# Kernel tuning notes

Measured on AMD Instinct MI355X. Metric: run time of the kernel, lower is better.

Reference implementation:

```python
import jax, jax.numpy as jnp
import numpy as np

N, E, DIN, H, HEADS = 50000, 800000, 128, 64, 4


def setup_inputs() -> dict:
    key = jax.random.key(0)
    ks = jax.random.split(key, 12)

    def p(k, shape, fan_in):
        return jax.random.normal(k, shape, dtype=jnp.float32) / np.float32(np.sqrt(fan_in))

    return dict(
        x=jax.random.normal(ks[0], (N, DIN), dtype=jnp.float32),
        edge_index=jax.random.randint(ks[1], (2, E), 0, N, dtype=jnp.int32),
        # GCNConv(input_dim, hidden)
        W_gcn=p(ks[2], (DIN, H), DIN), b_gcn=jnp.zeros((H,), jnp.float32),
        # GATConv(hidden, hidden, heads=4, concat=True)
        W_gat=p(ks[3], (H, HEADS * H), H),
        att_src=p(ks[4], (HEADS, H), H), att_dst=p(ks[5], (HEADS, H), H),
        b_gat=jnp.zeros((HEADS * H,), jnp.float32),
        # SAGEConv(4*hidden, hidden): lin_l (neighbors, with bias), lin_r (root, no bias)
        W_sage_l=p(ks[6], (HEADS * H, H), HEADS * H), b_sage=jnp.zeros((H,), jnp.float32),
        W_sage_r=p(ks[7], (HEADS * H, H), HEADS * H),
        # edge-pair MLP: Linear(2*hidden, hidden) -> ReLU -> Linear(hidden, 1)
        W1=p(ks[8], (2 * H, H), 2 * H), b1=jnp.zeros((H,), jnp.float32),
        W2=p(ks[9], (H, 1), H), b2=jnp.zeros((1,), jnp.float32),
    )


def reference(x, edge_index, W_gcn, b_gcn, W_gat, att_src, att_dst, b_gat,
              W_sage_l, b_sage, W_sage_r, W1, b1, W2, b2):
    n = x.shape[0]
    src, dst = edge_index[0], edge_index[1]
    loop = jnp.arange(n, dtype=edge_index.dtype)
    # edges with self-loops appended (GCN and GAT add self-loops by default)
    s2 = jnp.concatenate([src, loop])
    d2 = jnp.concatenate([dst, loop])

    h = x @ W_gcn                                            # [N, H]
    deg = jax.ops.segment_sum(jnp.ones_like(d2, jnp.float32), d2, num_segments=n)
    dinv = jnp.where(deg > 0, jax.lax.rsqrt(jnp.maximum(deg, 1e-12)), 0.0)
    norm = dinv[s2] * dinv[d2]                               # [E+N]
    h = jax.ops.segment_sum(h[s2] * norm[:, None], d2, num_segments=n) + b_gcn
    h = jax.nn.relu(h)                                       # dropout: identity in eval

    # ---- GATConv (heads=4, concat=True, negative_slope=0.2) ----
    g = (h @ W_gat).reshape(n, HEADS, H)                     # [N, heads, C]
    a_s = jnp.sum(g * att_src, axis=-1)                      # [N, heads]
    a_d = jnp.sum(g * att_dst, axis=-1)
    e = jax.nn.leaky_relu(a_s[s2] + a_d[d2], 0.2)            # [E+N, heads]
    m = jax.ops.segment_max(e, d2, num_segments=n)           # per-target max (stable softmax)
    e = jnp.exp(e - m[d2])
    z = jax.ops.segment_sum(e, d2, num_segments=n)
    alpha = e / (z[d2] + 1e-16)                              # edge softmax over incoming edges
    g = jax.ops.segment_sum(g[s2] * alpha[:, :, None], d2, num_segments=n)
    g = jax.nn.relu(g.reshape(n, HEADS * H) + b_gat)

    # ---- SAGEConv (mean aggregation, root weight, no self-loops) ----
    nsum = jax.ops.segment_sum(g[src], dst, num_segments=n)
    cnt = jax.ops.segment_sum(jnp.ones_like(dst, jnp.float32), dst, num_segments=n)
    mean = nsum / jnp.maximum(cnt, 1.0)[:, None]
    s = jax.nn.relu(mean @ W_sage_l + b_sage + g @ W_sage_r)  # [N, H]

    # ---- edge-pair MLP + sigmoid ----
    ef = jnp.concatenate([s[src], s[dst]], axis=1)            # [E, 2H]
    pred = jax.nn.relu(ef @ W1 + b1) @ W2 + b2                # [E, 1]
    return jax.nn.sigmoid(pred[:, 0])
```

## Files before the change

kernel.cpp:

```cpp
#include <hip/hip_runtime.h>
#include <math.h>

typedef float v2f __attribute__((ext_vector_type(2)));
static __device__ __forceinline__ float4 f4s(float v){ return make_float4(v,v,v,v); }
static __device__ __forceinline__ float4 f4add(float4 a, float4 b){ return make_float4(a.x+b.x,a.y+b.y,a.z+b.z,a.w+b.w); }
static __device__ __forceinline__ float4 f4max(float4 a, float4 b){ return make_float4(fmaxf(a.x,b.x),fmaxf(a.y,b.y),fmaxf(a.z,b.z),fmaxf(a.w,b.w)); }
static __device__ __forceinline__ float4 f4scale(float4 a, float s){ return make_float4(a.x*s,a.y*s,a.z*s,a.w*s); }
static __device__ __forceinline__ float4 f4fma(float4 acc, float s, float4 b){
  acc.x += s*b.x; acc.y += s*b.y; acc.z += s*b.z; acc.w += s*b.w; return acc;
}
static __device__ __forceinline__ float4 f4relu(float4 a){ return f4max(a, f4s(0.f)); }
static __device__ __forceinline__ float4 f4leaky(float4 a){
  return make_float4(a.x>0.f?a.x:0.2f*a.x, a.y>0.f?a.y:0.2f*a.y, a.z>0.f?a.z:0.2f*a.z, a.w>0.f?a.w:0.2f*a.w);
}
static __device__ __forceinline__ float4 f4expf(float4 a){ return make_float4(__expf(a.x),__expf(a.y),__expf(a.z),__expf(a.w)); }
static __device__ __forceinline__ unsigned short f2bf(float f){
  unsigned int u = __float_as_uint(f);
  unsigned int r = (u + 0x7fffu + ((u >> 16) & 1u)) >> 16;
  return (unsigned short)r;
}
static __device__ __forceinline__ ushort4 f2bf4(float4 f){
  ushort4 r; r.x=f2bf(f.x); r.y=f2bf(f.y); r.z=f2bf(f.z); r.w=f2bf(f.w); return r;
}
static __device__ __forceinline__ float4 bfu2f4(uint2 u){
  return make_float4(__uint_as_float(u.x << 16), __uint_as_float(u.x & 0xffff0000u),
                     __uint_as_float(u.y << 16), __uint_as_float(u.y & 0xffff0000u));
}
static __device__ __forceinline__ float4 bfu2f4_lo(uint4 u){ return bfu2f4(make_uint2(u.x, u.y)); }
static __device__ __forceinline__ float4 bfu2f4_hi(uint4 u){ return bfu2f4(make_uint2(u.z, u.w)); }

typedef __attribute__((ext_vector_type(8))) unsigned short u16x8;
static __device__ __forceinline__ u16x8 f2bf8(float4 a, float4 b){
  u16x8 r;
  r[0]=f2bf(a.x); r[1]=f2bf(a.y); r[2]=f2bf(a.z); r[3]=f2bf(a.w);
  r[4]=f2bf(b.x); r[5]=f2bf(b.y); r[6]=f2bf(b.z); r[7]=f2bf(b.w);
  return r;
}
static __device__ __forceinline__ void red2(float4& a, float4& b){
  a.x += __shfl_xor(a.x, 8); a.y += __shfl_xor(a.y, 8);
  a.z += __shfl_xor(a.z, 8); a.w += __shfl_xor(a.w, 8);
  b.x += __shfl_xor(b.x, 8); b.y += __shfl_xor(b.y, 8);
  b.z += __shfl_xor(b.z, 8); b.w += __shfl_xor(b.w, 8);
}
static __device__ __forceinline__ unsigned char f2fp8(float v){
  return (unsigned char)(__builtin_amdgcn_cvt_pk_fp8_f32(v, v, 0, false) & 0xff);
}
static __device__ __forceinline__ unsigned int f4_fp8x4(float4 v){
  unsigned int r = __builtin_amdgcn_cvt_pk_fp8_f32(v.x, v.y, 0, false);
  r = __builtin_amdgcn_cvt_pk_fp8_f32(v.z, v.w, r, true);
  return r;
}
static __device__ __forceinline__ float4 fp8x4_f4(unsigned int q){
  v2f lo = __builtin_amdgcn_cvt_pk_f32_fp8(q, false);
  v2f hi = __builtin_amdgcn_cvt_pk_f32_fp8(q, true);
  return make_float4(lo[0], lo[1], hi[0], hi[1]);
}
static __device__ __forceinline__ float dot8(float4 a, float4 b, const float* v){
  return a.x*v[0]+a.y*v[1]+a.z*v[2]+a.w*v[3]+b.x*v[4]+b.y*v[5]+b.z*v[6]+b.w*v[7];
}

typedef __attribute__((ext_vector_type(8))) short bf16x8;
typedef __attribute__((ext_vector_type(4))) float f32x4;

__global__ __launch_bounds__(256) void k_rankw(const int* __restrict__ dst, int* __restrict__ cnt,
                                               int* __restrict__ rank, int E, int fb,
                                               const float* __restrict__ Wg, const float* __restrict__ Wl,
                                               const float* __restrict__ Wr, unsigned short* __restrict__ WT){
  if ((int)blockIdx.x < fb){
    int t = blockIdx.x*256 + threadIdx.x;
    if (t < E) rank[t] = atomicAdd(&cnt[dst[t]], 1);
    return;
  }
  int s = (blockIdx.x - fb)*256 + threadIdx.x;
  int l = s & 63, f = s >> 6;
  const float* wp; int ld;
  if (s < 2048){
    int cc = f & 15, kb = f >> 4;
    int c  = cc*16 + (l & 15);
    int kr = kb*32 + ((l >> 4) << 3);
    wp = Wg + (size_t)kr*256 + c; ld = 256;
  } else {
    int f2 = f - 32;
    int cc = f2 & 7, kb = f2 >> 3;
    int c  = cc*16 + (l & 15);
    int kr = kb*32 + ((l >> 4) << 3);
    wp = (c >= 64) ? (Wr + (size_t)kr*64 + (c - 64)) : (Wl + (size_t)kr*64 + c);
    ld = 64;
  }
  u16x8 o;
  #pragma unroll
  for (int j = 0; j < 8; ++j) o[j] = f2bf(wp[(size_t)j*ld]);
  *(u16x8*)(WT + (size_t)s*8) = o;
}

__global__ __launch_bounds__(256) void k_scan1v(const int* __restrict__ cnt, int* __restrict__ excl,
                                                int* __restrict__ bsum, int n, int nb,
                                                const float* __restrict__ Wg, const float* __restrict__ as,
                                                const float* __restrict__ ad, float* __restrict__ Vs,
                                                float* __restrict__ Vd){
  if ((int)blockIdx.x == nb){
    int t = threadIdx.x;
    int h = t >> 6, k = t & 63;
    float s = 0.f, d = 0.f;
    const float* wr = Wg + (size_t)k*256 + h*64;
    const float* ar = as + h*64;
    const float* dr = ad + h*64;
    for (int c = 0; c < 64; ++c){ float w = wr[c]; s += w*ar[c]; d += w*dr[c]; }
    Vs[t] = s; Vd[t] = d;
    return;
  }
  __shared__ int sc[256];
  int t = threadIdx.x; int i = blockIdx.x*256 + t;
  int v = (i<n)?cnt[i]:0;
  sc[t]=v; __syncthreads();
  for (int o=1;o<256;o<<=1){ int a=(t>=o)?sc[t-o]:0; __syncthreads(); sc[t]+=a; __syncthreads(); }
  if (i<n) excl[i] = sc[t]-v;
  if (t==255) bsum[blockIdx.x] = sc[t];
}
__global__ __launch_bounds__(256) void k_scan3b(const int* __restrict__ cnt, const int* __restrict__ excl,
                                                const int* __restrict__ bsum, int* __restrict__ offs,
                                                float* __restrict__ dinv, int n, int E, int nb){
  __shared__ int sb[256];
  int t = threadIdx.x;
  int v = (t<nb)?bsum[t]:0;
  sb[t]=v; __syncthreads();
  for (int o=1;o<256;o<<=1){ int a=(t>=o)?sb[t-o]:0; __syncthreads(); sb[t]+=a; __syncthreads(); }
  int bex = sb[blockIdx.x] - bsum[blockIdx.x];
  int i = blockIdx.x*256 + t;
  if (i < n){
    offs[i] = excl[i] + bex;
    dinv[i] = rsqrtf((float)cnt[i] + 1.0f);
    if (i == 0) offs[n] = E;
  }
}

__global__ __launch_bounds__(256) void k_fillg(const int* __restrict__ src, const int* __restrict__ dstv,
                                               const int* __restrict__ offs, const int* __restrict__ rank,
                                               int* __restrict__ csr, int E, int fb,
                                               const float* __restrict__ x, const float* __restrict__ Wg,
                                               unsigned char* __restrict__ a8, int n,
                                               const float* __restrict__ dinv){
  if ((int)blockIdx.x < fb){
    int t = blockIdx.x*256 + threadIdx.x;
    if (t < E) csr[offs[dstv[t]] + rank[t]] = src[t];
    return;
  }
  __shared__ unsigned short wb[1024*8];
  int tid = threadIdx.x;
  for (int s = tid; s < 1024; s += 256){
    int l = s & 63, f = s >> 6;
    int cc = f & 3, kb = f >> 2;
    int c  = cc*16 + (l & 15);
    int kr = kb*32 + ((l >> 4) << 3);
    const float* wp = Wg + (size_t)kr*64 + c;
    unsigned short* dp = &wb[s*8];
    #pragma unroll
    for (int j = 0; j < 8; ++j) dp[j] = f2bf(wp[(size_t)j*64]);
  }
  __syncthreads();
  int wv = tid >> 6, l = tid & 63;
  int lrow = l & 15;
  int lk = (l >> 4) << 3;
  int g = blockIdx.x - fb;
  int r0 = (g << 6) + (wv << 4);
  int m = r0 + lrow;
  bf16x8 afr[4];
  #pragma unroll
  for (int kb = 0; kb < 4; ++kb){
    bf16x8 a = {0,0,0,0,0,0,0,0};
    if (m < n){
      const float* p = x + (size_t)m*128 + kb*32 + lk;
      float4 f0 = *(const float4*)p;
      float4 f1 = *(const float4*)(p + 4);
      a[0]=(short)f2bf(f0.x); a[1]=(short)f2bf(f0.y); a[2]=(short)f2bf(f0.z); a[3]=(short)f2bf(f0.w);
      a[4]=(short)f2bf(f1.x); a[5]=(short)f2bf(f1.y); a[6]=(short)f2bf(f1.z); a[7]=(short)f2bf(f1.w);
    }
    afr[kb] = a;
  }
  int rbase = r0 + ((l >> 4) << 2);
  float sc[4];
  #pragma unroll
  for (int r = 0; r < 4; ++r) sc[r] = (rbase + r < n) ? dinv[rbase + r] : 0.f;
  #pragma unroll
  for (int cc = 0; cc < 4; ++cc){
    f32x4 acc = {0.f, 0.f, 0.f, 0.f};
    #pragma unroll
    for (int kb = 0; kb < 4; ++kb){
      bf16x8 b = *(const bf16x8*)&wb[((kb*4 + cc)*64 + l)*8];
      acc = __builtin_amdgcn_mfma_f32_16x16x32_bf16(afr[kb], b, acc, 0, 0, 0);
    }
    int c = cc*16 + lrow;
    #pragma unroll
    for (int r = 0; r < 4; ++r){
      int rr = rbase + r;
      if (rr < n) a8[(size_t)rr*64 + c] = f2fp8(acc[r] * sc[r]);
    }
  }
}

__global__ __launch_bounds__(256) void k_gcn(const unsigned char* __restrict__ a8, const float* __restrict__ dinv,
                                             const float* __restrict__ b, const int* __restrict__ offs,
                                             const int* __restrict__ csr, const float* __restrict__ Vs,
                                             const float* __restrict__ Vd, unsigned char* __restrict__ h8,
                                             float* __restrict__ D, int n){
  __shared__ float svs[256], svd[256];
  svs[threadIdx.x] = Vs[threadIdx.x];
  svd[threadIdx.x] = Vd[threadIdx.x];
  __syncthreads();
  int l = threadIdx.x & 63;
  int node = (((blockIdx.x*256 + threadIdx.x) >> 6) << 2) + (l >> 4);
  int l15 = l & 15;
  int grp = l15 >> 3, sub = l15 & 7;
  bool ok = node < n;
  int beg = 0, end = 0;
  float di = 0.f;
  if (ok){ beg = offs[node]; end = offs[node+1]; di = dinv[node]; }
  float4 aL0 = f4s(0.f), aH0 = f4s(0.f), aL1 = f4s(0.f), aH1 = f4s(0.f);
  int i = beg + grp;
  for (; i + 2 < end; i += 4){
    int s0 = csr[i], s1 = csr[i+2];
    uint2 u0 = *(const uint2*)(a8 + (size_t)s0*64 + (sub<<3));
    uint2 u1 = *(const uint2*)(a8 + (size_t)s1*64 + (sub<<3));
    aL0 = f4add(aL0, fp8x4_f4(u0.x)); aH0 = f4add(aH0, fp8x4_f4(u0.y));
    aL1 = f4add(aL1, fp8x4_f4(u1.x)); aH1 = f4add(aH1, fp8x4_f4(u1.y));
  }
  if (i < end){
    int s0 = csr[i];
    uint2 u0 = *(const uint2*)(a8 + (size_t)s0*64 + (sub<<3));
    aL0 = f4add(aL0, fp8x4_f4(u0.x)); aH0 = f4add(aH0, fp8x4_f4(u0.y));
  }
  float4 aL = f4add(aL0, aL1), aH = f4add(aH0, aH1);
  red2(aL, aH);
  if (ok){
    uint2 us = *(const uint2*)(a8 + (size_t)node*64 + (sub<<3));
    aL = f4add(aL, fp8x4_f4(us.x)); aH = f4add(aH, fp8x4_f4(us.y));
    float4 b0 = *(const float4*)(b + (sub<<3));
    float4 b1 = *(const float4*)(b + (sub<<3) + 4);
    float4 r0 = f4relu(f4fma(b0, di, aL));
    float4 r1 = f4relu(f4fma(b1, di, aH));
    if (grp == 0){
      uint2 q; q.x = f4_fp8x4(r0); q.y = f4_fp8x4(r1);
      *(uint2*)(h8 + (size_t)node*64 + (sub<<3)) = q;
    }
    const float* vs0 = svs + (grp*128) + (sub<<3);
    const float* vd0 = svd + (grp*128) + (sub<<3);
    float s0 = dot8(r0, r1, vs0);
    float s1 = dot8(r0, r1, vs0 + 64);
    float d0 = dot8(r0, r1, vd0);
    float d1 = dot8(r0, r1, vd0 + 64);
    #pragma unroll
    for (int o = 1; o < 8; o <<= 1){
      s0 += __shfl_xor(s0, o); s1 += __shfl_xor(s1, o);
      d0 += __shfl_xor(d0, o); d1 += __shfl_xor(d1, o);
    }
    if (sub == 0){
      *(float2*)(D + (size_t)node*8 + grp*2)     = make_float2(s0, s1);
      *(float2*)(D + (size_t)node*8 + 4 + grp*2) = make_float2(d0, d1);
    }
  }
}

#define GAT_CAP 128
__global__ __launch_bounds__(256) void k_gat2f(const float* __restrict__ D, const unsigned char* __restrict__ H8,
                                               const int* __restrict__ offs, const int* __restrict__ csr,
                                               const unsigned short* __restrict__ WT, const float* __restrict__ bg,
                                               unsigned short* __restrict__ R, unsigned char* __restrict__ P8, int n){
  __shared__ __align__(16) unsigned char smem_raw[8*GAT_CAP*4*4 + 8*GAT_CAP*4];
  __shared__ unsigned short ytile[32][264];
  float (*wl)[GAT_CAP*4] = reinterpret_cast<float (*)[GAT_CAP*4]>(smem_raw);
  int   (*sl)[GAT_CAP]   = reinterpret_cast<int (*)[GAT_CAP]>(smem_raw + 8*GAT_CAP*4*4);
  unsigned short* gtile  = reinterpret_cast<unsigned short*>(smem_raw);
  const unsigned short* WT1 = WT;
  const unsigned short* WT2 = WT + 2048*8;
  int tid = threadIdx.x;
  int hw = tid >> 5;
  int l5 = tid & 31;
  int grp = l5 >> 4;
  int sub = l5 & 15;
  for (int batch = 0; batch < 4; ++batch){
    int lrow32 = batch*8 + hw;
    int node = blockIdx.x*32 + lrow32;
    if (node < n){
      int beg = offs[node], end = offs[node+1];
      int deg = end - beg;
      float4 ed  = *(const float4*)(D + (size_t)node*8 + 4);
      float4 es0 = *(const float4*)(D + (size_t)node*8);
      float4 wself = f4expf(f4leaky(f4add(es0, ed)));
      float4 z4 = f4s(0.f);
      for (int i = beg + l5; i < end; i += 32){
        int s = csr[i];
        float4 w = f4expf(f4leaky(f4add(*(const float4*)(D + (size_t)s*8), ed)));
        int li = i - beg;
        if (li < GAT_CAP){ *(float4*)&wl[hw][li<<2] = w; sl[hw][li] = s << 6; }
        z4 = f4add(z4, w);
      }
      for (int m = 1; m < 32; m <<= 1){
        z4.x += __shfl_xor(z4.x, m); z4.y += __shfl_xor(z4.y, m);
        z4.z += __shfl_xor(z4.z, m); z4.w += __shfl_xor(z4.w, m);
      }
      z4 = f4add(z4, wself);
      int c0b = sub << 2;
      float4 a0 = f4s(0.f), a1 = f4s(0.f), a2 = f4s(0.f), a3 = f4s(0.f);
      int nl = deg < GAT_CAP ? deg : GAT_CAP;
      int i = grp;
      for (; i + 2 < nl; i += 4){
        int o0 = sl[hw][i], o1 = sl[hw][i+2];
        float4 w0 = *(const float4*)&wl[hw][i<<2];
        float4 w1 = *(const float4*)&wl[hw][(i+2)<<2];
        unsigned int q0 = *(const unsigned int*)(H8 + o0 + c0b);
        unsigned int q1 = *(const unsigned int*)(H8 + o1 + c0b);
        float4 f0 = fp8x4_f4(q0);
        float4 f1 = fp8x4_f4(q1);
        a0 = f4fma(a0, w0.x, f0); a1 = f4fma(a1, w0.y, f0);
        a2 = f4fma(a2, w0.z, f0); a3 = f4fma(a3, w0.w, f0);
        a0 = f4fma(a0, w1.x, f1); a1 = f4fma(a1, w1.y, f1);
        a2 = f4fma(a2, w1.z, f1); a3 = f4fma(a3, w1.w, f1);
      }
      if (i < nl){
        float4 w0 = *(const float4*)&wl[hw][i<<2];
        float4 f0 = fp8x4_f4(*(const unsigned int*)(H8 + sl[hw][i] + c0b));
        a0 = f4fma(a0, w0.x, f0); a1 = f4fma(a1, w0.y, f0);
        a2 = f4fma(a2, w0.z, f0); a3 = f4fma(a3, w0.w, f0);
      }
      for (int j = nl + grp; j < deg; j += 2){
        int s = csr[beg+j];
        float4 e = f4leaky(f4add(*(const float4*)(D + (size_t)s*8), ed));
        float4 w = f4expf(e);
        float4 f0 = fp8x4_f4(*(const unsigned int*)(H8 + ((size_t)s << 6) + c0b));
        a0 = f4fma(a0, w.x, f0); a1 = f4fma(a1, w.y, f0);
        a2 = f4fma(a2, w.z, f0); a3 = f4fma(a3, w.w, f0);
      }
      a0.x += __shfl_xor(a0.x, 16); a0.y += __shfl_xor(a0.y, 16); a0.z += __shfl_xor(a0.z, 16); a0.w += __shfl_xor(a0.w, 16);
      a1.x += __shfl_xor(a1.x, 16); a1.y += __shfl_xor(a1.y, 16); a1.z += __shfl_xor(a1.z, 16); a1.w += __shfl_xor(a1.w, 16);
      a2.x += __shfl_xor(a2.x, 16); a2.y += __shfl_xor(a2.y, 16); a2.z += __shfl_xor(a2.z, 16); a2.w += __shfl_xor(a2.w, 16);
      a3.x += __shfl_xor(a3.x, 16); a3.y += __shfl_xor(a3.y, 16); a3.z += __shfl_xor(a3.z, 16); a3.w += __shfl_xor(a3.w, 16);
      if (grp == 0){
        float4 fs = fp8x4_f4(*(const unsigned int*)(H8 + ((size_t)node << 6) + c0b));
        a0 = f4fma(a0, wself.x, fs);
        a1 = f4fma(a1, wself.y, fs);
        a2 = f4fma(a2, wself.z, fs);
        a3 = f4fma(a3, wself.w, fs);
        a0 = f4scale(a0, 1.f/(z4.x + 1e-16f));
        a1 = f4scale(a1, 1.f/(z4.y + 1e-16f));
        a2 = f4scale(a2, 1.f/(z4.z + 1e-16f));
        a3 = f4scale(a3, 1.f/(z4.w + 1e-16f));
        unsigned short* yp = &ytile[lrow32][sub << 2];
        *(ushort4*)(yp)       = f2bf4(a0);
        *(ushort4*)(yp + 64)  = f2bf4(a1);
        *(ushort4*)(yp + 128) = f2bf4(a2);
        *(ushort4*)(yp + 192) = f2bf4(a3);
      }
    } else if (grp == 0){
      ushort4 z = make_ushort4(0,0,0,0);
      unsigned short* yp = &ytile[lrow32][sub << 2];
      *(ushort4*)(yp)       = z;
      *(ushort4*)(yp + 64)  = z;
      *(ushort4*)(yp + 128) = z;
      *(ushort4*)(yp + 192) = z;
    }
  }
  __syncthreads();
  int wv = tid >> 6, l = tid & 63;
  int lrow = l & 15;
  int lk = (l >> 4) << 3;
  int rbase4 = (l >> 4) << 2;
  bf16x8 afA[2][2];
  #pragma unroll
  for (int t = 0; t < 2; ++t){
    afA[t][0] = *(const bf16x8*)&ytile[t*16 + lrow][wv*64 + lk];
    afA[t][1] = *(const bf16x8*)&ytile[t*16 + lrow][wv*64 + 32 + lk];
  }
  #pragma unroll
  for (int q = 0; q < 4; ++q){
    int cc = wv*4 + q;
    bf16x8 b0 = *(const bf16x8*)&WT1[((size_t)((0*16 + cc)*64 + l))*8];
    bf16x8 b1 = *(const bf16x8*)&WT1[((size_t)((1*16 + cc)*64 + l))*8];
    int c = cc*16 + lrow;
    float bv = bg[c];
    #pragma unroll
    for (int t = 0; t < 2; ++t){
      f32x4 acc = {0.f, 0.f, 0.f, 0.f};
      acc = __builtin_amdgcn_mfma_f32_16x16x32_bf16(afA[t][0], b0, acc, 0, 0, 0);
      acc = __builtin_amdgcn_mfma_f32_16x16x32_bf16(afA[t][1], b1, acc, 0, 0, 0);
      #pragma unroll
      for (int r = 0; r < 4; ++r)
        gtile[(t*16 + rbase4 + r)*264 + c] = f2bf(fmaxf(acc[r] + bv, 0.f));
    }
  }
  __syncthreads();
  bf16x8 afb[2][8];
  #pragma unroll
  for (int t = 0; t < 2; ++t)
    #pragma unroll
    for (int kb = 0; kb < 8; ++kb)
      afb[t][kb] = *(const bf16x8*)&gtile[(t*16 + lrow)*264 + kb*32 + lk];
  #pragma unroll
  for (int q = 0; q < 2; ++q){
    int cc = wv*2 + q;
    f32x4 acc0 = {0.f, 0.f, 0.f, 0.f};
    f32x4 acc1 = {0.f, 0.f, 0.f, 0.f};
    #pragma unroll
    for (int kb = 0; kb < 8; ++kb){
      bf16x8 b = *(const bf16x8*)&WT2[((size_t)((kb*8 + cc)*64 + l))*8];
      acc0 = __builtin_amdgcn_mfma_f32_16x16x32_bf16(afb[0][kb], b, acc0, 0, 0, 0);
      acc1 = __builtin_amdgcn_mfma_f32_16x16x32_bf16(afb[1][kb], b, acc1, 0, 0, 0);
    }
    int c = cc*16 + lrow;
    #pragma unroll
    for (int t = 0; t < 2; ++t){
      const f32x4& acc = t ? acc1 : acc0;
      #pragma unroll
      for (int r = 0; r < 4; ++r){
        int nd = blockIdx.x*32 + t*16 + rbase4 + r;
        if (nd < n){
          float v = acc[r];
          if (c < 64) P8[(size_t)nd*64 + c] = f2fp8(v);
          else        R[(size_t)nd*64 + (c - 64)] = f2bf(v);
        }
      }
    }
  }
}

__global__ __launch_bounds__(256) void k_sage(const unsigned char* __restrict__ P8, const unsigned short* __restrict__ R,
                                              const float* __restrict__ b, const int* __restrict__ offs,
                                              const int* __restrict__ csr, const float* __restrict__ W1a,
                                              const float* __restrict__ W1b, unsigned char* __restrict__ T2, int n){
  __shared__ unsigned short wfr[1024*8];
  __shared__ unsigned short stile[16][72];
  int tid = threadIdx.x;
  for (int s = tid; s < 1024; s += 256){
    int l = s & 63, f = s >> 6;
    int cc = f & 7, kb = f >> 3;
    int c  = cc*16 + (l & 15);
    int kr = kb*32 + ((l >> 4) << 3);
    const float* wp = (c >= 64) ? (W1b + (size_t)kr*64 + (c - 64)) : (W1a + (size_t)kr*64 + c);
    unsigned short* dp = &wfr[s*8];
    #pragma unroll
    for (int j = 0; j < 8; ++j) dp[j] = f2bf(wp[(size_t)j*64]);
  }
  int wv = tid >> 6, l = tid & 63;
  int base = blockIdx.x*16;
  int lrow16 = (wv << 2) + (l >> 4);
  int node = base + lrow16;
  int l15 = l & 15;
  int grp = l15 >> 3, sub = l15 & 7;
  bool ok = node < n;
  int beg = 0, end = 0;
  if (ok){ beg = offs[node]; end = offs[node+1]; }
  float4 aL0 = f4s(0.f), aH0 = f4s(0.f), aL1 = f4s(0.f), aH1 = f4s(0.f);
  int i = beg + grp;
  for (; i + 2 < end; i += 4){
    int s0 = csr[i], s1 = csr[i+2];
    uint2 u0 = *(const uint2*)(P8 + (size_t)s0*64 + (sub<<3));
    uint2 u1 = *(const uint2*)(P8 + (size_t)s1*64 + (sub<<3));
    aL0 = f4add(aL0, fp8x4_f4(u0.x)); aH0 = f4add(aH0, fp8x4_f4(u0.y));
    aL1 = f4add(aL1, fp8x4_f4(u1.x)); aH1 = f4add(aH1, fp8x4_f4(u1.y));
  }
  if (i < end){
    int s0 = csr[i];
    uint2 u0 = *(const uint2*)(P8 + (size_t)s0*64 + (sub<<3));
    aL0 = f4add(aL0, fp8x4_f4(u0.x)); aH0 = f4add(aH0, fp8x4_f4(u0.y));
  }
  float4 aL = f4add(aL0, aL1), aH = f4add(aH0, aH1);
  red2(aL, aH);
  float4 r0 = f4s(0.f), r1 = f4s(0.f);
  if (ok){
    float minv = 1.f / fmaxf((float)(end - beg), 1.f);
    uint4 ur = *(const uint4*)(R + (size_t)node*64 + (sub<<3));
    float4 b0 = *(const float4*)(b + (sub<<3));
    float4 b1 = *(const float4*)(b + (sub<<3) + 4);
    r0 = f4relu(f4add(f4fma(b0, minv, aL), bfu2f4_lo(ur)));
    r1 = f4relu(f4add(f4fma(b1, minv, aH), bfu2f4_hi(ur)));
  }
  if (grp == 0) *(u16x8*)&stile[lrow16][sub << 3] = f2bf8(r0, r1);
  __syncthreads();
  int lrow = l & 15, lk = (l >> 4) << 3;
  bf16x8 af0 = *(const bf16x8*)&stile[lrow][lk];
  bf16x8 af1 = *(const bf16x8*)&stile[lrow][32 + lk];
  int rbase = (l >> 4) << 2;
  #pragma unroll
  for (int q = 0; q < 2; ++q){
    int cc = wv*2 + q;
    f32x4 acc = {0.f, 0.f, 0.f, 0.f};
    acc = __builtin_amdgcn_mfma_f32_16x16x32_bf16(af0, *(const bf16x8*)&wfr[(cc*64 + l)*8], acc, 0, 0, 0);
    acc = __builtin_amdgcn_mfma_f32_16x16x32_bf16(af1, *(const bf16x8*)&wfr[((8 + cc)*64 + l)*8], acc, 0, 0, 0);
    int c = cc*16 + lrow;
    #pragma unroll
    for (int r = 0; r < 4; ++r){
      int nd = base + rbase + r;
      if (nd < n) T2[(size_t)nd*128 + c] = f2fp8(acc[r]);
    }
  }
}

__global__ __launch_bounds__(256) void k_mlp(const unsigned char* __restrict__ T2,
                                             const float* __restrict__ b1, const float* __restrict__ W2,
                                             const float* __restrict__ b2, const int* __restrict__ src,
                                             const int* __restrict__ dst, float* __restrict__ out, int E){
  int t = threadIdx.x;
  int e = blockIdx.x*32 + (t >> 3);
  if (e >= E) return;
  int sub = t & 7;
  int s = src[e], d = dst[e];
  uint2 uu = *(const uint2*)(T2 + (size_t)s*128 + (sub<<3));
  uint2 vv = *(const uint2*)(T2 + (size_t)d*128 + 64 + (sub<<3));
  float4 u0 = fp8x4_f4(uu.x), u1 = fp8x4_f4(uu.y);
  float4 v0 = fp8x4_f4(vv.x), v1 = fp8x4_f4(vv.y);
  float4 bb0 = *(const float4*)(b1 + (sub<<3));
  float4 bb1 = *(const float4*)(b1 + (sub<<3) + 4);
  float4 w0 = *(const float4*)(W2 + (sub<<3));
  float4 w1 = *(const float4*)(W2 + (sub<<3) + 4);
  float4 ta = f4relu(f4add(f4add(u0, v0), bb0));
  float4 tb = f4relu(f4add(f4add(u1, v1), bb1));
  float p = ta.x*w0.x + ta.y*w0.y + ta.z*w0.z + ta.w*w0.w
          + tb.x*w1.x + tb.y*w1.y + tb.z*w1.z + tb.w*w1.w;
  p += __shfl_xor(p, 1);
  p += __shfl_xor(p, 2);
  p += __shfl_xor(p, 4);
  if (sub == 0) out[e] = 1.f / (1.f + __expf(-(p + b2[0])));
}

extern "C" void kernel_launch(void* const* d_in, const int* in_sizes, int n_in,
                              void* d_out, int out_size, void* d_ws, size_t ws_size,
                              hipStream_t stream){
  const float* x     = (const float*)d_in[0];
  const int*   eidx  = (const int*)  d_in[1];
  const float* W_gcn = (const float*)d_in[2];
  const float* b_gcn = (const float*)d_in[3];
  const float* W_gat = (const float*)d_in[4];
  const float* att_s = (const float*)d_in[5];
  const float* att_d = (const float*)d_in[6];
  const float* b_gat = (const float*)d_in[7];
  const float* W_sl  = (const float*)d_in[8];
  const float* b_sg  = (const float*)d_in[9];
  const float* W_sr  = (const float*)d_in[10];
  const float* W1    = (const float*)d_in[11];
  const float* b1    = (const float*)d_in[12];
  const float* W2    = (const float*)d_in[13];
  const float* b2    = (const float*)d_in[14];
  float* out = (float*)d_out;

  const int N = in_sizes[0] / 128;
  const int E = in_sizes[1] / 2;
  const int* src = eidx;
  const int* dst = eidx + E;

  float* ws   = (float*)d_ws;
  float* dinv = ws;
  float* D    = dinv + (size_t)N;
  float* Vs   = D + (size_t)N*8;
  float* Vd   = Vs + 256;
  unsigned short* WT = (unsigned short*)(Vd + 256);
  unsigned short* R  = WT + (size_t)6144*8;
  unsigned char*  A8 = (unsigned char*)(R + (size_t)N*64);
  unsigned char*  H8 = A8 + (size_t)N*64;
  unsigned char*  P8 = H8 + (size_t)N*64;
  unsigned char*  T2 = P8 + (size_t)N*64;
  int* cnt  = (int*)(T2 + (size_t)N*128);
  int* excl = cnt + N;
  int* bsum = excl + N;
  int* offs = bsum + 256;
  int* rank = offs + N + 1;
  int* csr  = rank + E;

  const int nb = (N + 255) / 256;
  const int fb = (E + 255) / 256;
  const int gtiles = (N + 63) / 64;
  const int nwb = (N + 15) / 16;

  hipMemsetAsync(cnt, 0, (size_t)N*sizeof(int), stream);
  k_rankw <<<fb + 24, 256, 0, stream>>>(dst, cnt, rank, E, fb, W_gat, W_sl, W_sr, WT);
  k_scan1v<<<nb + 1, 256, 0, stream>>>(cnt, excl, bsum, N, nb, W_gat, att_s, att_d, Vs, Vd);
  k_scan3b<<<nb, 256, 0, stream>>>(cnt, excl, bsum, offs, dinv, N, E, nb);
  k_fillg <<<fb + gtiles, 256, 0, stream>>>(src, dst, offs, rank, csr, E, fb,
                                            x, W_gcn, A8, N, dinv);

  k_gcn <<<nwb, 256, 0, stream>>>(A8, dinv, b_gcn, offs, csr, Vs, Vd, H8, D, N);

  k_gat2f<<<(N+31)/32, 256, 0, stream>>>(D, H8, offs, csr, WT, b_gat, R, P8, N);

  k_sage<<<nwb, 256, 0, stream>>>(P8, R, b_sg, offs, csr, W1, W1 + 64*64, T2, N);

  k_mlp <<<(E+31)/32, 256, 0, stream>>>(T2, b1, W2, b2, src, dst, out, E);
}
```

Before: 272.0 us.

## Precompute MLP weight fragments once and shrink GAT shared memory footprint

After: 279.9 us. +2.9%, slower.

```diff
diff --git a/kernel.cpp b/kernel.cpp
--- a/kernel.cpp
+++ b/kernel.cpp
@@ -65,7 +65,8 @@
 __global__ __launch_bounds__(256) void k_rankw(const int* __restrict__ dst, int* __restrict__ cnt,
                                                int* __restrict__ rank, int E, int fb,
                                                const float* __restrict__ Wg, const float* __restrict__ Wl,
-                                               const float* __restrict__ Wr, unsigned short* __restrict__ WT){
+                                               const float* __restrict__ Wr, const float* __restrict__ W1a,
+                                               const float* __restrict__ W1b, unsigned short* __restrict__ WT){
   if ((int)blockIdx.x < fb){
     int t = blockIdx.x*256 + threadIdx.x;
     if (t < E) rank[t] = atomicAdd(&cnt[dst[t]], 1);
@@ -79,12 +80,19 @@
     int c  = cc*16 + (l & 15);
     int kr = kb*32 + ((l >> 4) << 3);
     wp = Wg + (size_t)kr*256 + c; ld = 256;
-  } else {
+  } else if (s < 6144){
     int f2 = f - 32;
     int cc = f2 & 7, kb = f2 >> 3;
     int c  = cc*16 + (l & 15);
     int kr = kb*32 + ((l >> 4) << 3);
     wp = (c >= 64) ? (Wr + (size_t)kr*64 + (c - 64)) : (Wl + (size_t)kr*64 + c);
+    ld = 64;
+  } else {
+    int f3 = f - 96;
+    int cc = f3 & 7, kb = f3 >> 3;
+    int c  = cc*16 + (l & 15);
+    int kr = kb*32 + ((l >> 4) << 3);
+    wp = (c >= 64) ? (W1b + (size_t)kr*64 + (c - 64)) : (W1a + (size_t)kr*64 + c);
     ld = 64;
   }
   u16x8 o;
@@ -265,11 +273,8 @@
                                                const int* __restrict__ offs, const int* __restrict__ csr,
                                                const unsigned short* __restrict__ WT, const float* __restrict__ bg,
                                                unsigned short* __restrict__ R, unsigned char* __restrict__ P8, int n){
-  __shared__ __align__(16) unsigned char smem_raw[8*GAT_CAP*4*4 + 8*GAT_CAP*4];
+  __shared__ int sl[8][GAT_CAP];
   __shared__ unsigned short ytile[32][264];
-  float (*wl)[GAT_CAP*4] = reinterpret_cast<float (*)[GAT_CAP*4]>(smem_raw);
-  int   (*sl)[GAT_CAP]   = reinterpret_cast<int (*)[GAT_CAP]>(smem_raw + 8*GAT_CAP*4*4);
-  unsigned short* gtile  = reinterpret_cast<unsigned short*>(smem_raw);
   const unsigned short* WT1 = WT;
   const unsigned short* WT2 = WT + 2048*8;
   int tid = threadIdx.x;
@@ -291,7 +296,7 @@
         int s = csr[i];
         float4 w = f4expf(f4leaky(f4add(*(const float4*)(D + (size_t)s*8), ed)));
         int li = i - beg;
-        if (li < GAT_CAP){ *(float4*)&wl[hw][li<<2] = w; sl[hw][li] = s << 6; }
+        if (li < GAT_CAP) sl[hw][li] = s << 6;
         z4 = f4add(z4, w);
       }
       for (int m = 1; m < 32; m <<= 1){
@@ -305,10 +310,12 @@
       int i = grp;
       for (; i + 2 < nl; i += 4){
         int o0 = sl[hw][i], o1 = sl[hw][i+2];
-        float4 w0 = *(const float4*)&wl[hw][i<<2];
-        float4 w1 = *(const float4*)&wl[hw][(i+2)<<2];
+        float4 e0 = *(const float4*)(D + ((size_t)(o0 >> 6))*8);
+        float4 e1 = *(const float4*)(D + ((size_t)(o1 >> 6))*8);
         unsigned int q0 = *(const unsigned int*)(H8 + o0 + c0b);
         unsigned int q1 = *(const unsigned int*)(H8 + o1 + c0b);
+        float4 w0 = f4expf(f4leaky(f4add(e0, ed)));
+        float4 w1 = f4expf(f4leaky(f4add(e1, ed)));
         float4 f0 = fp8x4_f4(q0);
         float4 f1 = fp8x4_f4(q1);
         a0 = f4fma(a0, w0.x, f0); a1 = f4fma(a1, w0.y, f0);
@@ -317,8 +324,11 @@
         a2 = f4fma(a2, w1.z, f1); a3 = f4fma(a3, w1.w, f1);
       }
       if (i < nl){
-        float4 w0 = *(const float4*)&wl[hw][i<<2];
-        float4 f0 = fp8x4_f4(*(const unsigned int*)(H8 + sl[hw][i] + c0b));
+        int o0 = sl[hw][i];
+        float4 e0 = *(const float4*)(D + ((size_t)(o0 >> 6))*8);
+        unsigned int q0 = *(const unsigned int*)(H8 + o0 + c0b);
+        float4 w0 = f4expf(f4leaky(f4add(e0, ed)));
+        float4 f0 = fp8x4_f4(q0);
         a0 = f4fma(a0, w0.x, f0); a1 = f4fma(a1, w0.y, f0);
         a2 = f4fma(a2, w0.z, f0); a3 = f4fma(a3, w0.w, f0);
       }
@@ -384,7 +394,7 @@
       acc = __builtin_amdgcn_mfma_f32_16x16x32_bf16(afA[t][1], b1, acc, 0, 0, 0);
       #pragma unroll
       for (int r = 0; r < 4; ++r)
-        gtile[(t*16 + rbase4 + r)*264 + c] = f2bf(fmaxf(acc[r] + bv, 0.f));
+        ytile[t*16 + rbase4 + r][c] = f2bf(fmaxf(acc[r] + bv, 0.f));
     }
   }
   __syncthreads();
@@ -393,7 +403,7 @@
   for (int t = 0; t < 2; ++t)
     #pragma unroll
     for (int kb = 0; kb < 8; ++kb)
-      afb[t][kb] = *(const bf16x8*)&gtile[(t*16 + lrow)*264 + kb*32 + lk];
+      afb[t][kb] = *(const bf16x8*)&ytile[t*16 + lrow][kb*32 + lk];
   #pragma unroll
   for (int q = 0; q < 2; ++q){
     int cc = wv*2 + q;
@@ -424,21 +434,10 @@
 
 __global__ __launch_bounds__(256) void k_sage(const unsigned char* __restrict__ P8, const unsigned short* __restrict__ R,
                                               const float* __restrict__ b, const int* __restrict__ offs,
-                                              const int* __restrict__ csr, const float* __restrict__ W1a,
-                                              const float* __restrict__ W1b, unsigned char* __restrict__ T2, int n){
-  __shared__ unsigned short wfr[1024*8];
+                                              const int* __restrict__ csr, const unsigned short* __restrict__ WT3,
+                                              unsigned char* __restrict__ T2, int n){
   __shared__ unsigned short stile[16][72];
   int tid = threadIdx.x;
-  for (int s = tid; s < 1024; s += 256){
-    int l = s & 63, f = s >> 6;
-    int cc = f & 7, kb = f >> 3;
-    int c  = cc*16 + (l & 15);
-    int kr = kb*32 + ((l >> 4) << 3);
-    const float* wp = (c >= 64) ? (W1b + (size_t)kr*64 + (c - 64)) : (W1a + (size_t)kr*64 + c);
-    unsigned short* dp = &wfr[s*8];
-    #pragma unroll
-    for (int j = 0; j < 8; ++j) dp[j] = f2bf(wp[(size_t)j*64]);
-  }
   int wv = tid >> 6, l = tid & 63;
   int base = blockIdx.x*16;
   int lrow16 = (wv << 2) + (l >> 4);
@@ -483,8 +482,8 @@
   for (int q = 0; q < 2; ++q){
     int cc = wv*2 + q;
     f32x4 acc = {0.f, 0.f, 0.f, 0.f};
-    acc = __builtin_amdgcn_mfma_f32_16x16x32_bf16(af0, *(const bf16x8*)&wfr[(cc*64 + l)*8], acc, 0, 0, 0);
-    acc = __builtin_amdgcn_mfma_f32_16x16x32_bf16(af1, *(const bf16x8*)&wfr[((8 + cc)*64 + l)*8], acc, 0, 0, 0);
+    acc = __builtin_amdgcn_mfma_f32_16x16x32_bf16(af0, *(const bf16x8*)&WT3[((size_t)((0*8 + cc)*64 + l))*8], acc, 0, 0, 0);
+    acc = __builtin_amdgcn_mfma_f32_16x16x32_bf16(af1, *(const bf16x8*)&WT3[((size_t)((1*8 + cc)*64 + l))*8], acc, 0, 0, 0);
     int c = cc*16 + lrow;
     #pragma unroll
     for (int r = 0; r < 4; ++r){
@@ -552,7 +551,7 @@
   float* Vs   = D + (size_t)N*8;
   float* Vd   = Vs + 256;
   unsigned short* WT = (unsigned short*)(Vd + 256);
-  unsigned short* R  = WT + (size_t)6144*8;
+  unsigned short* R  = WT + (size_t)7168*8;
   unsigned char*  A8 = (unsigned char*)(R + (size_t)N*64);
   unsigned char*  H8 = A8 + (size_t)N*64;
   unsigned char*  P8 = H8 + (size_t)N*64;
@@ -570,7 +569,8 @@
   const int nwb = (N + 15) / 16;
 
   hipMemsetAsync(cnt, 0, (size_t)N*sizeof(int), stream);
-  k_rankw <<<fb + 24, 256, 0, stream>>>(dst, cnt, rank, E, fb, W_gat, W_sl, W_sr, WT);
+  k_rankw <<<fb + 28, 256, 0, stream>>>(dst, cnt, rank, E, fb, W_gat, W_sl, W_sr,
+                                        W1, W1 + 64*64, WT);
   k_scan1v<<<nb + 1, 256, 0, stream>>>(cnt, excl, bsum, N, nb, W_gat, att_s, att_d, Vs, Vd);
   k_scan3b<<<nb, 256, 0, stream>>>(cnt, excl, bsum, offs, dinv, N, E, nb);
   k_fillg <<<fb + gtiles, 256, 0, stream>>>(src, dst, offs, rank, csr, E, fb,
@@ -580,7 +580,7 @@
 
   k_gat2f<<<(N+31)/32, 256, 0, stream>>>(D, H8, offs, csr, WT, b_gat, R, P8, N);
 
-  k_sage<<<nwb, 256, 0, stream>>>(P8, R, b_sg, offs, csr, W1, W1 + 64*64, T2, N);
+  k_sage<<<nwb, 256, 0, stream>>>(P8, R, b_sg, offs, csr, WT + (size_t)6144*8, T2, N);
 
   k_mlp <<<(E+31)/32, 256, 0, stream>>>(T2, b1, W2, b2, src, dst, out, E);
 }
```
